# Kernel optimization log

Measured on AMD Instinct MI355X. Metric: run time of the kernel, lower is better.

## Reference

```python
import jax, jax.numpy as jnp
import numpy as np

C = 512
CD = C // 8  # query/key channel dim
EPS = 1e-5


def conv1x1(x, W, b):
    # x: [B,C,H,W], W: [Cout,Cin], b: [Cout]
    return jnp.einsum('bchw,dc->bdhw', x, W) + b[None, :, None, None]


def criss_cross(x, Wq, bq, Wk, bk, Wv, bv, gamma):
    B, Cc, H, Wd = x.shape
    q = conv1x1(x, Wq, bq)   # [B,CD,H,W]
    k = conv1x1(x, Wk, bk)   # [B,CD,H,W]
    v = conv1x1(x, Wv, bv)   # [B,C,H,W]
    # column (height) path energies: e_H[b,h,w,g] = <q[:, :,h,w], k[:,:,g,w]>
    e_h = jnp.einsum('bdhw,bdgw->bhwg', q, k)
    diag = jnp.eye(H, dtype=bool)[:, None, :]          # [H,1,H] over (h,g)
    e_h = jnp.where(diag[None], -jnp.inf, e_h)          # -inf on self position (CCNet INF mask)
    # row (width) path energies: e_w[b,h,w,v] = <q[:,:,h,w], k[:,:,h,v]>
    e_w = jnp.einsum('bdhw,bdhv->bhwv', q, k)
    att = jax.nn.softmax(jnp.concatenate([e_h, e_w], axis=-1), axis=-1)  # [B,H,W,H+W]
    a_h, a_w = att[..., :H], att[..., H:]
    out_h = jnp.einsum('bhwg,bcgw->bchw', a_h, v)
    out_w = jnp.einsum('bhwv,bchv->bchw', a_w, v)
    return gamma * (out_h + out_w) + x


def batchnorm2d(x, w, b):
    mean = jnp.mean(x, axis=(0, 2, 3), keepdims=True)
    var = jnp.var(x, axis=(0, 2, 3), keepdims=True)  # biased variance (training-mode BN)
    return (x - mean) * jax.lax.rsqrt(var + EPS) * w[None, :, None, None] + b[None, :, None, None]


def setup_inputs() -> dict:
    key = jax.random.key(0)
    ks = jax.random.split(key, 9)
    B, H, W = 8, 96, 96
    s_in = 1.0 / np.sqrt(C)
    return {
        'x': jax.random.normal(ks[0], (B, C, H, W), dtype=jnp.float32),
        'Wq': jax.random.normal(ks[1], (CD, C), dtype=jnp.float32) * s_in,
        'bq': jax.random.normal(ks[2], (CD,), dtype=jnp.float32) * 0.01,
        'Wk': jax.random.normal(ks[3], (CD, C), dtype=jnp.float32) * s_in,
        'bk': jax.random.normal(ks[4], (CD,), dtype=jnp.float32) * 0.01,
        'Wv': jax.random.normal(ks[5], (C, C), dtype=jnp.float32) * s_in,
        'bv': jax.random.normal(ks[6], (C,), dtype=jnp.float32) * 0.01,
        'gamma': jnp.float32(0.5),
        'bn_weight': jnp.ones((C,), dtype=jnp.float32) + 0.1 * jax.random.normal(ks[7], (C,), dtype=jnp.float32),
        'bn_bias': 0.1 * jax.random.normal(ks[8], (C,), dtype=jnp.float32),
        'recurrent': 2,
    }


def reference(x, Wq, bq, Wk, bk, Wv, bv, gamma, bn_weight, bn_bias, recurrent):
    for _ in range(recurrent):
        x = criss_cross(x, Wq, bq, Wk, bk, Wv, bv, gamma)
    return batchnorm2d(x, bn_weight, bn_bias)
```

## Files before the change

### kernel.cpp

```cpp
#include <hip/hip_runtime.h>
#include <math.h>


typedef short s16x8 __attribute__((ext_vector_type(8)));
typedef short s16x4 __attribute__((ext_vector_type(4)));
typedef float f32x4 __attribute__((ext_vector_type(4)));
typedef unsigned short us;

namespace {
constexpr int kB = 8;
constexpr int kC = 512;
constexpr int kH = 96;
constexpr int kW = 96;
constexpr int kHW = kH * kW;
constexpr int kN = kB * kHW;
}

__device__ inline us f2bf(float f) {
  union { float f; unsigned u; } v;
  v.f = f;
  const unsigned r = v.u + 0x7fffu + ((v.u >> 16) & 1u);
  return (us)(r >> 16);
}
__device__ inline float bf2f(us h) {
  union { unsigned u; float f; } v;
  v.u = ((unsigned)h) << 16;
  return v.f;
}

__global__ __launch_bounds__(256) void k_tr_in(const float* __restrict__ in,
                                               us* __restrict__ outb,
                                               us* __restrict__ outlo) {
  __shared__ float Lt[128][65];
  const int b = blockIdx.z;
  const int n0 = blockIdx.x * 128;
  const int c0 = blockIdx.y * 64;
  const int tid = threadIdx.x;
  {
    const int tx = tid & 31, cy = tid >> 5;
#pragma unroll
    for (int i = 0; i < 8; ++i) {
      const int cl = cy + 8 * i;
      const float4 v =
          *(const float4*)&in[((size_t)b * kC + c0 + cl) * kHW + n0 + 4 * tx];
      Lt[4 * tx + 0][cl] = v.x;
      Lt[4 * tx + 1][cl] = v.y;
      Lt[4 * tx + 2][cl] = v.z;
      Lt[4 * tx + 3][cl] = v.w;
    }
  }
  __syncthreads();
  {
    const int cq = tid & 15, nl = tid >> 4;
#pragma unroll
    for (int p = 0; p < 8; ++p) {
      const int n = nl + 16 * p;
      s16x4 hi4, lo4;
#pragma unroll
      for (int j = 0; j < 4; ++j) {
        const float f = Lt[n][4 * cq + j];
        const us h = f2bf(f);
        hi4[j] = (short)h;
        lo4[j] = (short)f2bf(f - bf2f(h));
      }
      const size_t o = ((size_t)b * kHW + n0 + n) * kC + c0 + 4 * cq;
      *(s16x4*)&outb[o] = hi4;
      *(s16x4*)&outlo[o] = lo4;
    }
  }
}

__global__ __launch_bounds__(256) void k_cvt_wqk(const float* __restrict__ Wq,
                                                 const float* __restrict__ Wk,
                                                 us* __restrict__ whi,
                                                 us* __restrict__ wlo) {
  const int i = blockIdx.x * 256 + threadIdx.x;
  const int m = i >> 9, c = i & 511;
  const float v = m < 64 ? Wq[m * kC + c] : Wk[(m - 64) * kC + c];
  const us hi = f2bf(v);
  whi[i] = hi;
  wlo[i] = f2bf(v - bf2f(hi));
}
__global__ __launch_bounds__(256) void k_cvt_wv(const float* __restrict__ Wv,
                                                us* __restrict__ wvb) {
  const int i = blockIdx.x * 256 + threadIdx.x;
  wvb[i] = f2bf(Wv[i]);
}

__global__ __launch_bounds__(256) void k_gemm_qk(
    const us* __restrict__ xtb, const us* __restrict__ xtlo,
    const us* __restrict__ whi, const us* __restrict__ wlo,
    const float* __restrict__ bq, const float* __restrict__ bk,
    us* __restrict__ qkh, us* __restrict__ qkl) {
  __shared__ __align__(16) us AsH[128 * 64];
  __shared__ __align__(16) us AsL[128 * 64];
  __shared__ __align__(16) us BsH[128 * 64];
  __shared__ __align__(16) us BsL[128 * 64];
  const int bid = blockIdx.x;
  const int n0 = ((bid & 7) * 72 + (bid >> 3)) * 128;
  const int tid = threadIdx.x, lane = tid & 63;
  const int wr = (tid >> 6) >> 1, wc = (tid >> 6) & 1;
  const int l15 = lane & 15, kg = lane >> 4;
  f32x4 acc[4][4] = {};
  for (int kk = 0; kk < kC; kk += 64) {
    __syncthreads();
#pragma unroll
    for (int p = 0; p < 4; ++p) {
      const int idx = p * 256 + tid;
      const int r = idx >> 3, c8 = idx & 7;
      const int cs = (c8 ^ (r & 7)) * 8;
      const int db = (p * 256 + (tid & 192)) * 8;
      const size_t ga = (size_t)(n0 + r) * kC + kk + cs;
      const size_t gb = (size_t)r * kC + kk + cs;
      __builtin_amdgcn_global_load_lds((const unsigned*)&xtb[ga],
                                       (unsigned*)&AsH[db], 16, 0, 0);
      __builtin_amdgcn_global_load_lds((const unsigned*)&xtlo[ga],
                                       (unsigned*)&AsL[db], 16, 0, 0);
      __builtin_amdgcn_global_load_lds((const unsigned*)&whi[gb],
                                       (unsigned*)&BsH[db], 16, 0, 0);
      __builtin_amdgcn_global_load_lds((const unsigned*)&wlo[gb],
                                       (unsigned*)&BsL[db], 16, 0, 0);
    }
    __syncthreads();
#pragma unroll
    for (int ks = 0; ks < 2; ++ks) {
      s16x8 ah[4], al[4], bh[4], bl[4];
#pragma unroll
      for (int mf = 0; mf < 4; ++mf) {
        const int r = wr * 64 + mf * 16 + l15;
        const int off = r * 64 + (((ks * 4 + kg) ^ (r & 7)) << 3);
        ah[mf] = *(const s16x8*)&AsH[off];
        al[mf] = *(const s16x8*)&AsL[off];
      }
#pragma unroll
      for (int nf = 0; nf < 4; ++nf) {
        const int r = wc * 64 + nf * 16 + l15;
        const int off = r * 64 + (((ks * 4 + kg) ^ (r & 7)) << 3);
        bh[nf] = *(const s16x8*)&BsH[off];
        bl[nf] = *(const s16x8*)&BsL[off];
      }
#pragma unroll
      for (int nf = 0; nf < 4; ++nf)
#pragma unroll
        for (int mf = 0; mf < 4; ++mf) {
          acc[nf][mf] = __builtin_amdgcn_mfma_f32_16x16x32_bf16(
              bh[nf], ah[mf], acc[nf][mf], 0, 0, 0);
          acc[nf][mf] = __builtin_amdgcn_mfma_f32_16x16x32_bf16(
              bh[nf], al[mf], acc[nf][mf], 0, 0, 0);
          acc[nf][mf] = __builtin_amdgcn_mfma_f32_16x16x32_bf16(
              bl[nf], ah[mf], acc[nf][mf], 0, 0, 0);
        }
    }
  }
#pragma unroll
  for (int nf = 0; nf < 4; ++nf) {
    const int mq = wc * 64 + nf * 16 + kg * 4;
    const f32x4 b4 = *(const f32x4*)((wc == 0) ? &bq[mq] : &bk[mq - 64]);
#pragma unroll
    for (int mf = 0; mf < 4; ++mf) {
      const int n = n0 + wr * 64 + mf * 16 + l15;
      const f32x4 v = acc[nf][mf] + b4;
      s16x4 hi4, lo4;
#pragma unroll
      for (int i = 0; i < 4; ++i) {
        const us h = f2bf(v[i]);
        hi4[i] = (short)h;
        lo4[i] = (short)f2bf(v[i] - bf2f(h));
      }
      *(s16x4*)&qkh[(size_t)n * 128 + mq] = hi4;
      *(s16x4*)&qkl[(size_t)n * 128 + mq] = lo4;
    }
  }
}

template <bool COL>
__global__ __launch_bounds__(256) void k_att(const us* __restrict__ qkh,
                                             const us* __restrict__ qkl,
                                             const us* __restrict__ xtb,
                                             us* __restrict__ aggxb,
                                             float2* __restrict__ ms) {
  __shared__ __align__(16) us QKs[4 * 96 * 72];
  __shared__ __align__(16) us Ps[96 * 104];
  __shared__ float2 al[96];
  us* Qh = QKs;
  us* Ql = QKs + 96 * 72;
  us* Kh = QKs + 2 * 96 * 72;
  us* Kl = QKs + 3 * 96 * 72;
  us* Xs = QKs;
  const int line = blockIdx.x;
  const int b = blockIdx.y;
  const int tid = threadIdx.x;
  const int lane = tid & 63, wave = tid >> 6, l15 = lane & 15, kg = lane >> 4;
  const size_t nbase = (size_t)b * kHW + (COL ? line : (size_t)line * kW);
  const size_t nstr = COL ? kW : 1;
  s16x8 xr[6];
#pragma unroll
  for (int u = 0; u < 6; ++u) {
    const int idx = tid + 256 * u;
    const int g = idx >> 4, c8 = idx & 15;
    xr[u] = *(const s16x8*)&xtb[(nbase + g * nstr) * kC + c8 * 8];
  }
#pragma unroll
  for (int u = 0; u < 6; ++u) {
    const int idx = tid + 256 * u;
    const int row = idx >> 4, seg = idx & 15;
    const size_t src = (nbase + row * nstr) * 128 + seg * 8;
    us* dh = (seg < 8 ? Qh : Kh) + row * 72 + (seg & 7) * 8;
    us* dl = (seg < 8 ? Ql : Kl) + row * 72 + (seg & 7) * 8;
    *(s16x8*)dh = *(const s16x8*)&qkh[src];
    *(s16x8*)dl = *(const s16x8*)&qkl[src];
  }
  __syncthreads();
  const int nrt = (wave < 2) ? 2 : 1;
  for (int rr = 0; rr < nrt; ++rr) {
    const int rt = wave + 4 * rr;
    f32x4 E[6] = {};
#pragma unroll
    for (int ks = 0; ks < 2; ++ks) {
      const int ko = ks * 32 + kg * 8;
      const s16x8 ah = *(const s16x8*)&Qh[(rt * 16 + l15) * 72 + ko];
      const s16x8 aq = *(const s16x8*)&Ql[(rt * 16 + l15) * 72 + ko];
#pragma unroll
      for (int ct = 0; ct < 6; ++ct) {
        const s16x8 bh = *(const s16x8*)&Kh[(ct * 16 + l15) * 72 + ko];
        const s16x8 bl = *(const s16x8*)&Kl[(ct * 16 + l15) * 72 + ko];
        E[ct] = __builtin_amdgcn_mfma_f32_16x16x32_bf16(ah, bh, E[ct], 0, 0, 0);
        E[ct] = __builtin_amdgcn_mfma_f32_16x16x32_bf16(ah, bl, E[ct], 0, 0, 0);
        E[ct] = __builtin_amdgcn_mfma_f32_16x16x32_bf16(aq, bh, E[ct], 0, 0, 0);
      }
    }
#pragma unroll
    for (int q = 0; q < 4; ++q) {
      const int row = rt * 16 + kg * 4 + q;
      if (COL && l15 == kg * 4 + q) E[rt][q] = -1e30f;
      float mx = E[0][q];
#pragma unroll
      for (int ct = 1; ct < 6; ++ct) mx = fmaxf(mx, E[ct][q]);
#pragma unroll
      for (int off = 1; off < 16; off <<= 1)
        mx = fmaxf(mx, __shfl_xor(mx, off, 64));
      float sm = 0.f;
#pragma unroll
      for (int ct = 0; ct < 6; ++ct) {
        const float e = __expf(E[ct][q] - mx);
        sm += e;
        Ps[row * 104 + ct * 16 + l15] = f2bf(e);
      }
#pragma unroll
      for (int off = 1; off < 16; off <<= 1) sm += __shfl_xor(sm, off, 64);
      if (l15 == 0) {
        if (COL) {
          ms[nbase + row * nstr] = make_float2(mx, sm);
        } else {
          const float2 mh = ms[nbase + row];
          const float M = fmaxf(mh.x, mx);
          const float eh = __expf(mh.x - M), ew = __expf(mx - M);
          const float S = mh.y * eh + sm * ew;
          al[row] = make_float2(eh / S, ew / S);
        }
      }
    }
  }
  __syncthreads();
  for (int cc = 0; cc < 4; ++cc) {
    const int c0 = cc * 128;
    s16x4 oldp[2][6];
    if (!COL) {
#pragma unroll
      for (int mf = 0; mf < 6; ++mf) {
        const size_t rb = (nbase + (mf * 16 + l15)) * kC;
#pragma unroll
        for (int nf = 0; nf < 2; ++nf)
          oldp[nf][mf] =
              *(const s16x4*)&aggxb[rb + c0 + (wave * 2 + nf) * 16 + kg * 4];
      }
    }
#pragma unroll
    for (int u = 0; u < 6; ++u) {
      const int idx = tid + 256 * u;
      const int g = idx >> 4, c8 = idx & 15;
#pragma unroll
      for (int i2 = 0; i2 < 8; ++i2) Xs[(c8 * 8 + i2) * 104 + g] = xr[u][i2];
    }
    if (cc < 3) {
#pragma unroll
      for (int u = 0; u < 6; ++u) {
        const int idx = tid + 256 * u;
        const int g = idx >> 4, c8 = idx & 15;
        xr[u] = *(const s16x8*)&xtb[(nbase + g * nstr) * kC + c0 + 128 + c8 * 8];
      }
    }
    __syncthreads();
    f32x4 acc[2][6] = {};
#pragma unroll
    for (int ks = 0; ks < 3; ++ks) {
      s16x8 xf[2], pf[6];
#pragma unroll
      for (int nf = 0; nf < 2; ++nf)
        xf[nf] = *(const s16x8*)
            &Xs[((wave * 2 + nf) * 16 + l15) * 104 + ks * 32 + kg * 8];
#pragma unroll
      for (int mf = 0; mf < 6; ++mf)
        pf[mf] = *(const s16x8*)&Ps[(mf * 16 + l15) * 104 + ks * 32 + kg * 8];
#pragma unroll
      for (int nf = 0; nf < 2; ++nf)
#pragma unroll
        for (int mf = 0; mf < 6; ++mf)
          acc[nf][mf] = __builtin_amdgcn_mfma_f32_16x16x32_bf16(
              xf[nf], pf[mf], acc[nf][mf], 0, 0, 0);
    }
#pragma unroll
    for (int mf = 0; mf < 6; ++mf) {
      const int pos = mf * 16 + l15;
      const size_t rb = (nbase + pos * nstr) * kC;
#pragma unroll
      for (int nf = 0; nf < 2; ++nf) {
        const int c = c0 + (wave * 2 + nf) * 16 + kg * 4;
        s16x4 st;
        if (COL) {
#pragma unroll
          for (int i = 0; i < 4; ++i) st[i] = (short)f2bf(acc[nf][mf][i]);
        } else {
          const float2 a2 = al[pos];
#pragma unroll
          for (int i = 0; i < 4; ++i)
            st[i] = (short)f2bf(a2.x * bf2f((us)oldp[nf][mf][i]) +
                                a2.y * acc[nf][mf][i]);
        }
        *(s16x4*)&aggxb[rb + c] = st;
      }
    }
    __syncthreads();
  }
}

template <bool LAST>
__global__ __launch_bounds__(512, 2) void k_proj_mfma(
    const us* __restrict__ aggxb, const us* __restrict__ wvb,
    const float* __restrict__ bv, const float* __restrict__ gammap,
    us* __restrict__ xtb, us* __restrict__ xtlo, float* __restrict__ stats) {
  __shared__ __align__(16) us As[2][256 * 64];
  __shared__ __align__(16) us Bs[2][256 * 64];
  __shared__ float bnS[256], bnQ[256];
  const int flat = blockIdx.x;
  const int swz = (flat & 7) * 72 + (flat >> 3);
  const int n0 = (swz >> 1) * 256;
  const int m0 = (swz & 1) * 256;
  const int tid = threadIdx.x, lane = tid & 63;
  const int wv = tid >> 6;
  const int wr = wv >> 2, wc = wv & 3;
  const int l15 = lane & 15, kg = lane >> 4;
  if (LAST && tid < 256) { bnS[tid] = 0.f; bnQ[tid] = 0.f; }

  auto stage = [&](int buf, int kk) {
#pragma unroll
    for (int p = 0; p < 4; ++p) {
      const int slot = p * 512 + tid;
      const int r = slot >> 3, c8 = slot & 7;
      const int cs = (c8 ^ (r & 7)) * 8;
      const int db = (p * 512 + (tid & 448)) * 8;
      __builtin_amdgcn_global_load_lds(
          (const unsigned*)&aggxb[(size_t)(n0 + r) * kC + kk + cs],
          (unsigned*)&As[buf][db], 16, 0, 0);
      __builtin_amdgcn_global_load_lds(
          (const unsigned*)&wvb[(size_t)(m0 + r) * kC + kk + cs],
          (unsigned*)&Bs[buf][db], 16, 0, 0);
    }
  };

  f32x4 acc[4][8] = {};
  stage(0, 0);
  __syncthreads();
  for (int t = 0; t < 8; ++t) {
    const int cur = t & 1;
    if (t < 7) stage(cur ^ 1, (t + 1) * 64);
#pragma unroll
    for (int ks = 0; ks < 2; ++ks) {
      s16x8 a[8], b[4];
#pragma unroll
      for (int mf = 0; mf < 8; ++mf) {
        const int r = wr * 128 + mf * 16 + l15;
        a[mf] = *(const s16x8*)&As[cur][r * 64 + (((ks * 4 + kg) ^ (r & 7)) << 3)];
      }
#pragma unroll
      for (int nf = 0; nf < 4; ++nf) {
        const int r = wc * 64 + nf * 16 + l15;
        b[nf] = *(const s16x8*)&Bs[cur][r * 64 + (((ks * 4 + kg) ^ (r & 7)) << 3)];
      }
#pragma unroll
      for (int nf = 0; nf < 4; ++nf)
#pragma unroll
        for (int mf = 0; mf < 8; ++mf)
          acc[nf][mf] = __builtin_amdgcn_mfma_f32_16x16x32_bf16(
              b[nf], a[mf], acc[nf][mf], 0, 0, 0);
    }
    __syncthreads();
  }
  const float g = gammap[0];
  float ps_[4][4], pq_[4][4];
  if (LAST) {
#pragma unroll
    for (int nf = 0; nf < 4; ++nf)
#pragma unroll
      for (int i = 0; i < 4; ++i) { ps_[nf][i] = 0.f; pq_[nf][i] = 0.f; }
  }
#pragma unroll
  for (int mf = 0; mf < 8; ++mf) {
    const int n = n0 + wr * 128 + mf * 16 + l15;
#pragma unroll
    for (int nf = 0; nf < 4; ++nf) {
      const int mq = m0 + wc * 64 + nf * 16 + kg * 4;
      const size_t o = (size_t)n * kC + mq;
      const f32x4 b4 = *(const f32x4*)&bv[mq];
      const s16x4 uh = *(const s16x4*)&xtb[o];
      const s16x4 ul = *(const s16x4*)&xtlo[o];
      s16x4 nh, nl;
#pragma unroll
      for (int i = 0; i < 4; ++i) {
        const float x = bf2f((us)uh[i]) + bf2f((us)ul[i]);
        const float r = g * (acc[nf][mf][i] + b4[i]) + x;
        const us hi = f2bf(r);
        nh[i] = (short)hi;
        nl[i] = (short)f2bf(r - bf2f(hi));
        if (LAST) { ps_[nf][i] += r; pq_[nf][i] += r * r; }
      }
      *(s16x4*)&xtb[o] = nh;
      *(s16x4*)&xtlo[o] = nl;
    }
  }
  if (LAST) {
#pragma unroll
    for (int nf = 0; nf < 4; ++nf)
#pragma unroll
      for (int i = 0; i < 4; ++i) {
        float s = ps_[nf][i], q = pq_[nf][i];
#pragma unroll
        for (int off = 1; off < 16; off <<= 1) {
          s += __shfl_xor(s, off, 64);
          q += __shfl_xor(q, off, 64);
        }
        if (l15 == 0) {
          const int cl = wc * 64 + nf * 16 + kg * 4 + i;
          atomicAdd(&bnS[cl], s);
          atomicAdd(&bnQ[cl], q);
        }
      }
    __syncthreads();
    if (tid < 256) {
      atomicAdd(&stats[m0 + tid], bnS[tid]);
      atomicAdd(&stats[kC + m0 + tid], bnQ[tid]);
    }
  }
}

__global__ __launch_bounds__(256) void k_bn_apply(
    const us* __restrict__ xtb, const us* __restrict__ xtlo,
    const float* __restrict__ stats, const float* __restrict__ bw,
    const float* __restrict__ bb, float* __restrict__ out) {
  __shared__ float Lt[128][65];
  __shared__ float sc[64], sh[64];
  const int b = blockIdx.z;
  const int n0 = blockIdx.x * 128;
  const int c0 = blockIdx.y * 64;
  const int tid = threadIdx.x;
  if (tid < 64) {
    const int c = c0 + tid;
    const float mean = stats[c] * (1.f / (float)kN);
    const float var = stats[kC + c] * (1.f / (float)kN) - mean * mean;
    const float r = rsqrtf(var + 1e-5f);
    sc[tid] = r * bw[c];
    sh[tid] = bb[c] - mean * r * bw[c];
  }
  __syncthreads();
  {
    const int cq = tid & 15, nl = tid >> 4;
#pragma unroll
    for (int p = 0; p < 8; ++p) {
      const int n = nl + 16 * p;
      const size_t o = ((size_t)b * kHW + n0 + n) * kC + c0 + 4 * cq;
      const s16x4 h4 = *(const s16x4*)&xtb[o];
      const s16x4 l4 = *(const s16x4*)&xtlo[o];
#pragma unroll
      for (int j = 0; j < 4; ++j) {
        const int c = 4 * cq + j;
        const float v = bf2f((us)h4[j]) + bf2f((us)l4[j]);
        Lt[n][c] = v * sc[c] + sh[c];
      }
    }
  }
  __syncthreads();
  {
    const int tx = tid & 31, cy = tid >> 5;
#pragma unroll
    for (int i = 0; i < 8; ++i) {
      const int cl = cy + 8 * i;
      float4 o4;
      o4.x = Lt[4 * tx + 0][cl];
      o4.y = Lt[4 * tx + 1][cl];
      o4.z = Lt[4 * tx + 2][cl];
      o4.w = Lt[4 * tx + 3][cl];
      *(float4*)&out[((size_t)b * kC + c0 + cl) * kHW + n0 + 4 * tx] = o4;
    }
  }
}

extern "C" void kernel_launch(void* const* d_in, const int* in_sizes, int n_in,
                              void* d_out, int out_size, void* d_ws,
                              size_t ws_size, hipStream_t stream) {
  const float* x_in = (const float*)d_in[0];
  const float* Wq = (const float*)d_in[1];
  const float* bq = (const float*)d_in[2];
  const float* Wk = (const float*)d_in[3];
  const float* bk = (const float*)d_in[4];
  const float* Wv = (const float*)d_in[5];
  const float* bv = (const float*)d_in[6];
  const float* gamma = (const float*)d_in[7];
  const float* bnw = (const float*)d_in[8];
  const float* bnb = (const float*)d_in[9];

  constexpr size_t NC = (size_t)kN * kC;
  us* xtb = (us*)d_ws;
  us* xtlo = xtb + NC;
  us* qkh = (us*)(xtlo + NC);
  us* qkl = qkh + (size_t)kN * 128;
  us* aggxb = qkl + (size_t)kN * 128;
  float2* ms = (float2*)(aggxb + NC);
  us* wqkhi = (us*)(ms + kN);
  us* wqklo = wqkhi + 128 * kC;
  us* wvb = wqklo + 128 * kC;
  float* stats = (float*)(wvb + kC * kC);

  k_tr_in<<<dim3(kHW / 128, kC / 64, kB), 256, 0, stream>>>(x_in, xtb, xtlo);
  k_cvt_wqk<<<dim3(128 * kC / 256), 256, 0, stream>>>(Wq, Wk, wqkhi, wqklo);
  k_cvt_wv<<<dim3(kC * kC / 256), 256, 0, stream>>>(Wv, wvb);
  hipMemsetAsync(stats, 0, 1024 * sizeof(float), stream);

  for (int it = 0; it < 2; ++it) {
    k_gemm_qk<<<dim3(kN / 128), 256, 0, stream>>>(xtb, xtlo, wqkhi, wqklo, bq,
                                                  bk, qkh, qkl);
    k_att<true><<<dim3(kW, kB), 256, 0, stream>>>(qkh, qkl, xtb, aggxb, ms);
    k_att<false><<<dim3(kH, kB), 256, 0, stream>>>(qkh, qkl, xtb, aggxb, ms);
    if (it == 0)
      k_proj_mfma<false><<<dim3((kN / 256) * 2), 512, 0, stream>>>(
          aggxb, wvb, bv, gamma, xtb, xtlo, stats);
    else
      k_proj_mfma<true><<<dim3((kN / 256) * 2), 512, 0, stream>>>(
          aggxb, wvb, bv, gamma, xtb, xtlo, stats);
  }

  k_bn_apply<<<dim3(kHW / 128, kC / 64, kB), 256, 0, stream>>>(
      xtb, xtlo, stats, bnw, bnb, (float*)d_out);
}
```

Measured before the change: 780.6 us.

## Fuse row attention with value projection and residual update per row

The templated attention kernel is split into a column-only kernel and a new row kernel. For each image row, the new kernel computes the row energies and softmax, merges them with the column result, keeps the aggregated features in LDS, and then runs the Wv projection, residual update and BN statistics itself. This removes the separate projection kernel and the global write and re-read of the aggregated tensor. In exchange, each block streams all of Wv from global memory without LDS staging. The projection tile is smaller (96 positions), and the large LDS footprint likely limits occupancy to one block per CU.

```diff
diff --git a/kernel.cpp b/kernel.cpp
--- a/kernel.cpp
+++ b/kernel.cpp
@@ -173,15 +173,13 @@
   }
 }
 
-template <bool COL>
-__global__ __launch_bounds__(256) void k_att(const us* __restrict__ qkh,
-                                             const us* __restrict__ qkl,
-                                             const us* __restrict__ xtb,
-                                             us* __restrict__ aggxb,
-                                             float2* __restrict__ ms) {
+__global__ __launch_bounds__(256) void k_att_col(const us* __restrict__ qkh,
+                                                 const us* __restrict__ qkl,
+                                                 const us* __restrict__ xtb,
+                                                 us* __restrict__ aggh,
+                                                 float2* __restrict__ ms) {
   __shared__ __align__(16) us QKs[4 * 96 * 72];
   __shared__ __align__(16) us Ps[96 * 104];
-  __shared__ float2 al[96];
   us* Qh = QKs;
   us* Ql = QKs + 96 * 72;
   us* Kh = QKs + 2 * 96 * 72;
@@ -191,8 +189,8 @@
   const int b = blockIdx.y;
   const int tid = threadIdx.x;
   const int lane = tid & 63, wave = tid >> 6, l15 = lane & 15, kg = lane >> 4;
-  const size_t nbase = (size_t)b * kHW + (COL ? line : (size_t)line * kW);
-  const size_t nstr = COL ? kW : 1;
+  const size_t nbase = (size_t)b * kHW + line;
+  const size_t nstr = kW;
   s16x8 xr[6];
 #pragma unroll
   for (int u = 0; u < 6; ++u) {
@@ -232,7 +230,7 @@
 #pragma unroll
     for (int q = 0; q < 4; ++q) {
       const int row = rt * 16 + kg * 4 + q;
-      if (COL && l15 == kg * 4 + q) E[rt][q] = -1e30f;
+      if (l15 == kg * 4 + q) E[rt][q] = -1e30f;
       float mx = E[0][q];
 #pragma unroll
       for (int ct = 1; ct < 6; ++ct) mx = fmaxf(mx, E[ct][q]);
@@ -248,33 +246,12 @@
       }
 #pragma unroll
       for (int off = 1; off < 16; off <<= 1) sm += __shfl_xor(sm, off, 64);
-      if (l15 == 0) {
-        if (COL) {
-          ms[nbase + row * nstr] = make_float2(mx, sm);
-        } else {
-          const float2 mh = ms[nbase + row];
-          const float M = fmaxf(mh.x, mx);
-          const float eh = __expf(mh.x - M), ew = __expf(mx - M);
-          const float S = mh.y * eh + sm * ew;
-          al[row] = make_float2(eh / S, ew / S);
-        }
-      }
+      if (l15 == 0) ms[nbase + row * nstr] = make_float2(mx, sm);
     }
   }
   __syncthreads();
   for (int cc = 0; cc < 4; ++cc) {
     const int c0 = cc * 128;
-    s16x4 oldp[2][6];
-    if (!COL) {
-#pragma unroll
-      for (int mf = 0; mf < 6; ++mf) {
-        const size_t rb = (nbase + (mf * 16 + l15)) * kC;
-#pragma unroll
-        for (int nf = 0; nf < 2; ++nf)
-          oldp[nf][mf] =
-              *(const s16x4*)&aggxb[rb + c0 + (wave * 2 + nf) * 16 + kg * 4];
-      }
-    }
 #pragma unroll
     for (int u = 0; u < 6; ++u) {
       const int idx = tid + 256 * u;
@@ -317,84 +294,185 @@
       for (int nf = 0; nf < 2; ++nf) {
         const int c = c0 + (wave * 2 + nf) * 16 + kg * 4;
         s16x4 st;
-        if (COL) {
-#pragma unroll
-          for (int i = 0; i < 4; ++i) st[i] = (short)f2bf(acc[nf][mf][i]);
-        } else {
-          const float2 a2 = al[pos];
-#pragma unroll
-          for (int i = 0; i < 4; ++i)
-            st[i] = (short)f2bf(a2.x * bf2f((us)oldp[nf][mf][i]) +
-                                a2.y * acc[nf][mf][i]);
+#pragma unroll
+        for (int i = 0; i < 4; ++i) st[i] = (short)f2bf(acc[nf][mf][i]);
+        *(s16x4*)&aggh[rb + c] = st;
+      }
+    }
+    __syncthreads();
+  }
+}
+
+template <bool LAST>
+__global__ __launch_bounds__(512, 2) void k_att_row_proj(
+    const us* __restrict__ qkh, const us* __restrict__ qkl,
+    const us* __restrict__ aggh, const float2* __restrict__ ms,
+    const us* __restrict__ wvb, const float* __restrict__ bv,
+    const float* __restrict__ gammap, us* __restrict__ xtb,
+    us* __restrict__ xtlo, float* __restrict__ stats) {
+  __shared__ __align__(16) us QK[2 * 96 * 72];
+  __shared__ __align__(16) us Ps[96 * 104];
+  __shared__ __align__(16) us aggP[96 * 520];
+  __shared__ float2 al[96];
+  us* Qs = QK;
+  us* Ks = QK + 96 * 72;
+  us* Xs = QK;
+  const int h = blockIdx.x;
+  const int b = blockIdx.y;
+  const int tid = threadIdx.x;
+  const int lane = tid & 63, wave = tid >> 6, l15 = lane & 15, kg = lane >> 4;
+  const size_t nbase = (size_t)b * kHW + (size_t)h * kW;
+
+  s16x8 xr[3];
+#pragma unroll
+  for (int u = 0; u < 3; ++u) {
+    const int idx = tid + 512 * u;
+    const int g = idx >> 4, c8 = idx & 15;
+    xr[u] = *(const s16x8*)&xtb[(nbase + g) * kC + c8 * 8];
+  }
+#pragma unroll
+  for (int u = 0; u < 3; ++u) {
+    const int idx = tid + 512 * u;
+    const int row = idx >> 4, seg = idx & 15;
+    us* d = (seg < 8 ? Qs : Ks) + row * 72 + (seg & 7) * 8;
+    *(s16x8*)d = *(const s16x8*)&qkh[(nbase + row) * 128 + seg * 8];
+  }
+  __syncthreads();
+  const int rt = wave;
+  f32x4 E[6] = {};
+  auto pass = [&]() {
+    if (wave < 6) {
+#pragma unroll
+      for (int ks = 0; ks < 2; ++ks) {
+        const int ko = ks * 32 + kg * 8;
+        const s16x8 a = *(const s16x8*)&Qs[(rt * 16 + l15) * 72 + ko];
+#pragma unroll
+        for (int ct = 0; ct < 6; ++ct) {
+          const s16x8 bfr = *(const s16x8*)&Ks[(ct * 16 + l15) * 72 + ko];
+          E[ct] = __builtin_amdgcn_mfma_f32_16x16x32_bf16(a, bfr, E[ct], 0, 0, 0);
         }
-        *(s16x4*)&aggxb[rb + c] = st;
+      }
+    }
+  };
+  pass();
+  __syncthreads();
+  for (int u = 0; u < 2; ++u) {
+    const int idx = tid + 512 * u;
+    if (idx < 768) {
+      const int row = idx >> 3, seg = idx & 7;
+      *(s16x8*)&Qs[row * 72 + seg * 8] =
+          *(const s16x8*)&qkl[(nbase + row) * 128 + seg * 8];
+    }
+  }
+  __syncthreads();
+  pass();
+  __syncthreads();
+#pragma unroll
+  for (int u = 0; u < 3; ++u) {
+    const int idx = tid + 512 * u;
+    const int row = idx >> 4, seg = idx & 15;
+    if (seg < 8)
+      *(s16x8*)&Qs[row * 72 + seg * 8] =
+          *(const s16x8*)&qkh[(nbase + row) * 128 + seg * 8];
+    else
+      *(s16x8*)&Ks[row * 72 + (seg - 8) * 8] =
+          *(const s16x8*)&qkl[(nbase + row) * 128 + seg * 8];
+  }
+  __syncthreads();
+  pass();
+  if (wave < 6) {
+#pragma unroll
+    for (int q = 0; q < 4; ++q) {
+      const int row = rt * 16 + kg * 4 + q;
+      float mx = E[0][q];
+#pragma unroll
+      for (int ct = 1; ct < 6; ++ct) mx = fmaxf(mx, E[ct][q]);
+#pragma unroll
+      for (int off = 1; off < 16; off <<= 1)
+        mx = fmaxf(mx, __shfl_xor(mx, off, 64));
+      float sm = 0.f;
+#pragma unroll
+      for (int ct = 0; ct < 6; ++ct) {
+        const float e = __expf(E[ct][q] - mx);
+        sm += e;
+        Ps[row * 104 + ct * 16 + l15] = f2bf(e);
+      }
+#pragma unroll
+      for (int off = 1; off < 16; off <<= 1) sm += __shfl_xor(sm, off, 64);
+      if (l15 == 0) {
+        const float2 mh = ms[nbase + row];
+        const float M = fmaxf(mh.x, mx);
+        const float eh = __expf(mh.x - M), ew = __expf(mx - M);
+        const float S = mh.y * eh + sm * ew;
+        al[row] = make_float2(eh / S, ew / S);
+      }
+    }
+  }
+  __syncthreads();
+  for (int cc = 0; cc < 4; ++cc) {
+    const int c0 = cc * 128;
+    s16x4 oldp[6];
+#pragma unroll
+    for (int mf = 0; mf < 6; ++mf)
+      oldp[mf] = *(const s16x4*)
+          &aggh[(nbase + mf * 16 + l15) * kC + c0 + wave * 16 + kg * 4];
+#pragma unroll
+    for (int u = 0; u < 3; ++u) {
+      const int idx = tid + 512 * u;
+      const int g = idx >> 4, c8 = idx & 15;
+#pragma unroll
+      for (int i2 = 0; i2 < 8; ++i2) Xs[(c8 * 8 + i2) * 104 + g] = xr[u][i2];
+    }
+    if (cc < 3) {
+#pragma unroll
+      for (int u = 0; u < 3; ++u) {
+        const int idx = tid + 512 * u;
+        const int g = idx >> 4, c8 = idx & 15;
+        xr[u] = *(const s16x8*)&xtb[(nbase + g) * kC + c0 + 128 + c8 * 8];
       }
     }
     __syncthreads();
-  }
-}
-
-template <bool LAST>
-__global__ __launch_bounds__(512, 2) void k_proj_mfma(
-    const us* __restrict__ aggxb, const us* __restrict__ wvb,
-    const float* __restrict__ bv, const float* __restrict__ gammap,
-    us* __restrict__ xtb, us* __restrict__ xtlo, float* __restrict__ stats) {
-  __shared__ __align__(16) us As[2][256 * 64];
-  __shared__ __align__(16) us Bs[2][256 * 64];
-  __shared__ float bnS[256], bnQ[256];
-  const int flat = blockIdx.x;
-  const int swz = (flat & 7) * 72 + (flat >> 3);
-  const int n0 = (swz >> 1) * 256;
-  const int m0 = (swz & 1) * 256;
-  const int tid = threadIdx.x, lane = tid & 63;
-  const int wv = tid >> 6;
-  const int wr = wv >> 2, wc = wv & 3;
-  const int l15 = lane & 15, kg = lane >> 4;
-  if (LAST && tid < 256) { bnS[tid] = 0.f; bnQ[tid] = 0.f; }
-
-  auto stage = [&](int buf, int kk) {
-#pragma unroll
-    for (int p = 0; p < 4; ++p) {
-      const int slot = p * 512 + tid;
-      const int r = slot >> 3, c8 = slot & 7;
-      const int cs = (c8 ^ (r & 7)) * 8;
-      const int db = (p * 512 + (tid & 448)) * 8;
-      __builtin_amdgcn_global_load_lds(
-          (const unsigned*)&aggxb[(size_t)(n0 + r) * kC + kk + cs],
-          (unsigned*)&As[buf][db], 16, 0, 0);
-      __builtin_amdgcn_global_load_lds(
-          (const unsigned*)&wvb[(size_t)(m0 + r) * kC + kk + cs],
-          (unsigned*)&Bs[buf][db], 16, 0, 0);
-    }
-  };
-
-  f32x4 acc[4][8] = {};
-  stage(0, 0);
-  __syncthreads();
-  for (int t = 0; t < 8; ++t) {
-    const int cur = t & 1;
-    if (t < 7) stage(cur ^ 1, (t + 1) * 64);
-#pragma unroll
-    for (int ks = 0; ks < 2; ++ks) {
-      s16x8 a[8], b[4];
-#pragma unroll
-      for (int mf = 0; mf < 8; ++mf) {
-        const int r = wr * 128 + mf * 16 + l15;
-        a[mf] = *(const s16x8*)&As[cur][r * 64 + (((ks * 4 + kg) ^ (r & 7)) << 3)];
-      }
-#pragma unroll
-      for (int nf = 0; nf < 4; ++nf) {
-        const int r = wc * 64 + nf * 16 + l15;
-        b[nf] = *(const s16x8*)&Bs[cur][r * 64 + (((ks * 4 + kg) ^ (r & 7)) << 3)];
-      }
-#pragma unroll
-      for (int nf = 0; nf < 4; ++nf)
-#pragma unroll
-        for (int mf = 0; mf < 8; ++mf)
-          acc[nf][mf] = __builtin_amdgcn_mfma_f32_16x16x32_bf16(
-              b[nf], a[mf], acc[nf][mf], 0, 0, 0);
+    f32x4 acc[6] = {};
+#pragma unroll
+    for (int ks = 0; ks < 3; ++ks) {
+      const s16x8 xf = *(const s16x8*)
+          &Xs[(wave * 16 + l15) * 104 + ks * 32 + kg * 8];
+#pragma unroll
+      for (int mf = 0; mf < 6; ++mf) {
+        const s16x8 pf =
+            *(const s16x8*)&Ps[(mf * 16 + l15) * 104 + ks * 32 + kg * 8];
+        acc[mf] = __builtin_amdgcn_mfma_f32_16x16x32_bf16(xf, pf, acc[mf], 0, 0, 0);
+      }
+    }
+#pragma unroll
+    for (int mf = 0; mf < 6; ++mf) {
+      const int pos = mf * 16 + l15;
+      const float2 a2 = al[pos];
+      const int c = c0 + wave * 16 + kg * 4;
+      s16x4 st;
+#pragma unroll
+      for (int i = 0; i < 4; ++i)
+        st[i] = (short)f2bf(a2.x * bf2f((us)oldp[mf][i]) + a2.y * acc[mf][i]);
+      *(s16x4*)&aggP[pos * 520 + c] = st;
     }
     __syncthreads();
+  }
+  f32x4 C[4][6] = {};
+  for (int k = 0; k < kC; k += 32) {
+    s16x8 bfr[4], afr[6];
+#pragma unroll
+    for (int nf = 0; nf < 4; ++nf)
+      bfr[nf] = *(const s16x8*)
+          &wvb[(size_t)(wave * 64 + nf * 16 + l15) * kC + k + kg * 8];
+#pragma unroll
+    for (int mf = 0; mf < 6; ++mf)
+      afr[mf] = *(const s16x8*)&aggP[(mf * 16 + l15) * 520 + k + kg * 8];
+#pragma unroll
+    for (int nf = 0; nf < 4; ++nf)
+#pragma unroll
+      for (int mf = 0; mf < 6; ++mf)
+        C[nf][mf] = __builtin_amdgcn_mfma_f32_16x16x32_bf16(
+            bfr[nf], afr[mf], C[nf][mf], 0, 0, 0);
   }
   const float g = gammap[0];
   float ps_[4][4], pq_[4][4];
@@ -405,12 +483,12 @@
       for (int i = 0; i < 4; ++i) { ps_[nf][i] = 0.f; pq_[nf][i] = 0.f; }
   }
 #pragma unroll
-  for (int mf = 0; mf < 8; ++mf) {
-    const int n = n0 + wr * 128 + mf * 16 + l15;
+  for (int mf = 0; mf < 6; ++mf) {
+    const size_t n = nbase + mf * 16 + l15;
 #pragma unroll
     for (int nf = 0; nf < 4; ++nf) {
-      const int mq = m0 + wc * 64 + nf * 16 + kg * 4;
-      const size_t o = (size_t)n * kC + mq;
+      const int mq = wave * 64 + nf * 16 + kg * 4;
+      const size_t o = n * kC + mq;
       const f32x4 b4 = *(const f32x4*)&bv[mq];
       const s16x4 uh = *(const s16x4*)&xtb[o];
       const s16x4 ul = *(const s16x4*)&xtlo[o];
@@ -418,7 +496,7 @@
 #pragma unroll
       for (int i = 0; i < 4; ++i) {
         const float x = bf2f((us)uh[i]) + bf2f((us)ul[i]);
-        const float r = g * (acc[nf][mf][i] + b4[i]) + x;
+        const float r = g * (C[nf][mf][i] + b4[i]) + x;
         const us hi = f2bf(r);
         nh[i] = (short)hi;
         nl[i] = (short)f2bf(r - bf2f(hi));
@@ -440,16 +518,11 @@
           q += __shfl_xor(q, off, 64);
         }
         if (l15 == 0) {
-          const int cl = wc * 64 + nf * 16 + kg * 4 + i;
-          atomicAdd(&bnS[cl], s);
-          atomicAdd(&bnQ[cl], q);
+          const int cl = wave * 64 + nf * 16 + kg * 4 + i;
+          atomicAdd(&stats[cl], s);
+          atomicAdd(&stats[kC + cl], q);
         }
       }
-    __syncthreads();
-    if (tid < 256) {
-      atomicAdd(&stats[m0 + tid], bnS[tid]);
-      atomicAdd(&stats[kC + m0 + tid], bnQ[tid]);
-    }
   }
 }
 
@@ -523,8 +596,8 @@
   us* xtlo = xtb + NC;
   us* qkh = (us*)(xtlo + NC);
   us* qkl = qkh + (size_t)kN * 128;
-  us* aggxb = qkl + (size_t)kN * 128;
-  float2* ms = (float2*)(aggxb + NC);
+  us* aggh = qkl + (size_t)kN * 128;
+  float2* ms = (float2*)(aggh + NC);
   us* wqkhi = (us*)(ms + kN);
   us* wqklo = wqkhi + 128 * kC;
   us* wvb = wqklo + 128 * kC;
@@ -538,14 +611,13 @@
   for (int it = 0; it < 2; ++it) {
     k_gemm_qk<<<dim3(kN / 128), 256, 0, stream>>>(xtb, xtlo, wqkhi, wqklo, bq,
                                                   bk, qkh, qkl);
-    k_att<true><<<dim3(kW, kB), 256, 0, stream>>>(qkh, qkl, xtb, aggxb, ms);
-    k_att<false><<<dim3(kH, kB), 256, 0, stream>>>(qkh, qkl, xtb, aggxb, ms);
+    k_att_col<<<dim3(kW, kB), 256, 0, stream>>>(qkh, qkl, xtb, aggh, ms);
     if (it == 0)
-      k_proj_mfma<false><<<dim3((kN / 256) * 2), 512, 0, stream>>>(
-          aggxb, wvb, bv, gamma, xtb, xtlo, stats);
+      k_att_row_proj<false><<<dim3(kH, kB), 512, 0, stream>>>(
+          qkh, qkl, aggh, ms, wvb, bv, gamma, xtb, xtlo, stats);
     else
-      k_proj_mfma<true><<<dim3((kN / 256) * 2), 512, 0, stream>>>(
-          aggxb, wvb, bv, gamma, xtb, xtlo, stats);
+      k_att_row_proj<true><<<dim3(kH, kB), 512, 0, stream>>>(
+          qkh, qkl, aggh, ms, wvb, bv, gamma, xtb, xtlo, stats);
   }
 
   k_bn_apply<<<dim3(kHW / 128, kC / 64, kB), 256, 0, stream>>>(
```

After: 790.4 us. Within noise of the previous version (+1.2%).
